# Performance work log

Measured on AMD Instinct MI355X. Metric: run time of the kernel, lower is better.

The kernel has to match this reference:

```python
import jax, jax.numpy as jnp
import numpy as np

EPS = 1e-07


def setup_inputs() -> dict:
    key = jax.random.key(0)
    k1, k2, k3 = jax.random.split(key, 3)
    B, T, R, F = 16, 512, 128, 32
    timesteps = jax.random.uniform(k1, (B, T, F), dtype=jnp.float32)          # observation times, > 0
    values = jax.random.normal(k2, (B, T, F), dtype=jnp.float32)              # observed values
    reference_timesteps = jax.random.uniform(k3, (B, R), dtype=jnp.float32)  # query times
    alpha = jnp.ones((1,), dtype=jnp.float32) * 50.0                          # learned bandwidth param (init a=50)
    return {"timesteps": timesteps, "values": values,
            "reference_timesteps": reference_timesteps, "alpha": alpha}


def reference(timesteps, values, reference_timesteps, alpha):
    # timesteps, values: [B, T, F]; reference_timesteps: [B, R]; alpha: [1]
    R = reference_timesteps.shape[1]
    t = timesteps[:, None, :, :]                       # [B, 1, T, F]
    r = reference_timesteps[:, :, None, None]          # [B, R, 1, 1]
    mask = (t > 0).astype(timesteps.dtype)             # [B, 1, T, F]
    # squared-exponential kernel with mask, normalized by R (as in intensity)
    dist = jnp.exp(-alpha[0] * (r - t) ** 2) * mask + EPS  # [B, R, T, F]
    dist = dist / R
    lam = dist.sum(axis=2)                             # [B, R, F]
    smooth = jnp.sum(dist * values[:, None, :, :], axis=2) / lam  # [B, R, F]
    return smooth
```

## Files before the change

kernel.cpp:

```cpp
#include <hip/hip_runtime.h>


constexpr int B_ = 16, T_ = 512, R_ = 128, F_ = 32;
constexpr int S_  = 4;
constexpr int TS_ = T_ / S_;
constexpr int RB_ = 8;
constexpr float EPS_ = 1e-7f;

__global__ __launch_bounds__(256) void ga_partial(
    const float* __restrict__ ts_g, const float* __restrict__ v_g,
    const float* __restrict__ ref_g, const float* __restrict__ alpha_g,
    float2* __restrict__ ws)
{
    __shared__ float tile[TS_ * F_ * 2];

    const int tid = threadIdx.x;
    const int s   = blockIdx.x % S_;
    const int rb  = (blockIdx.x / S_) % (R_ / RB_);
    const int b   = blockIdx.x / (S_ * (R_ / RB_));
    const int f   = tid & 31;
    const int rl  = tid >> 5;
    const int r_idx = rb * RB_ + rl;

    const float r    = ref_g[b * R_ + r_idx];
    const float nega = -alpha_g[0];

    const float4* tsg4 = (const float4*)(ts_g + (size_t)(b * T_ + s * TS_) * F_);
    const float4* vg4  = (const float4*)(v_g  + (size_t)(b * T_ + s * TS_) * F_);
    #pragma unroll
    for (int i = tid; i < TS_ * F_ / 4; i += 256) {
        float4 a = tsg4[i];
        float4 w = vg4[i];
        a.x = (a.x > 0.f) ? a.x : 2e19f;
        a.y = (a.y > 0.f) ? a.y : 2e19f;
        a.z = (a.z > 0.f) ? a.z : 2e19f;
        a.w = (a.w > 0.f) ? a.w : 2e19f;
        float4* dst = (float4*)(tile + 8 * i);
        dst[0] = make_float4(a.x, w.x, a.y, w.y);
        dst[1] = make_float4(a.z, w.z, a.w, w.w);
    }
    __syncthreads();

    const float2* t2 = (const float2*)tile;
    float num = 0.f, den = 0.f;
    #pragma unroll 8
    for (int t = 0; t < TS_; ++t) {
        float2 tv = t2[t * F_ + f];
        float d = r - tv.x;
        float e = __expf(nega * d * d);
        float wgt = e + EPS_;
        den += wgt;
        num = fmaf(wgt, tv.y, num);
    }

    ws[(size_t)s * (B_ * R_ * F_) + (size_t)(b * R_ + r_idx) * F_ + f] =
        make_float2(num, den);
}

__global__ __launch_bounds__(256) void ga_combine(
    const float2* __restrict__ ws, float* __restrict__ out)
{
    int i = blockIdx.x * 256 + threadIdx.x;
    float num = 0.f, den = 0.f;
    #pragma unroll
    for (int s = 0; s < S_; ++s) {
        float2 p = ws[(size_t)s * (B_ * R_ * F_) + i];
        num += p.x;
        den += p.y;
    }
    out[i] = num / den;
}

extern "C" void kernel_launch(void* const* d_in, const int* in_sizes, int n_in,
                              void* d_out, int out_size, void* d_ws, size_t ws_size,
                              hipStream_t stream) {
    const float* timesteps = (const float*)d_in[0];
    const float* values    = (const float*)d_in[1];
    const float* ref_ts    = (const float*)d_in[2];
    const float* alpha     = (const float*)d_in[3];
    float* out = (float*)d_out;
    float2* ws = (float2*)d_ws;

    ga_partial<<<B_ * (R_ / RB_) * S_, 256, 0, stream>>>(
        timesteps, values, ref_ts, alpha, ws);
    ga_combine<<<(B_ * R_ * F_) / 256, 256, 0, stream>>>(ws, out);
}
```

Measured before the change: 71.29 us.

## Fuse partial and combine kernels into one 1024-thread block per (b, r-block)

Replaces the two-kernel split-T scheme with a single kernel. Each 1024-thread block loads a full batch's T×F tile into LDS, and eight T-groups reduce their partial sums through shared memory before writing the output. It also computes two reference rows per thread to reuse each LDS load, packs two timesteps into a float4 read, and folds log2e into alpha so it can use exp2f. This removes the workspace round trip and the second launch, at the cost of a 128KB LDS tile, lower occupancy and fewer blocks (256).

```diff
diff --git a/kernel.cpp b/kernel.cpp
--- a/kernel.cpp
+++ b/kernel.cpp
@@ -2,73 +2,91 @@
 
 
 constexpr int B_ = 16, T_ = 512, R_ = 128, F_ = 32;
-constexpr int S_  = 4;
-constexpr int TS_ = T_ / S_;
-constexpr int RB_ = 8;
+constexpr int NTG = 8;
+constexpr int CT_ = T_ / NTG;
+constexpr int RSL = 4;
+constexpr int RB_ = RSL * 2;
 constexpr float EPS_ = 1e-7f;
+constexpr float LOG2E_ = 1.4426950408889634f;
 
-__global__ __launch_bounds__(256) void ga_partial(
+__global__ __launch_bounds__(1024) void ga_fused(
     const float* __restrict__ ts_g, const float* __restrict__ v_g,
     const float* __restrict__ ref_g, const float* __restrict__ alpha_g,
-    float2* __restrict__ ws)
+    float* __restrict__ out)
 {
-    __shared__ float tile[TS_ * F_ * 2];
+    __shared__ float4 tile[(T_ / 2) * F_];
 
     const int tid = threadIdx.x;
-    const int s   = blockIdx.x % S_;
-    const int rb  = (blockIdx.x / S_) % (R_ / RB_);
-    const int b   = blockIdx.x / (S_ * (R_ / RB_));
+    const int rb  = blockIdx.x & (R_ / RB_ - 1);
+    const int b   = blockIdx.x >> 4;
     const int f   = tid & 31;
-    const int rl  = tid >> 5;
-    const int r_idx = rb * RB_ + rl;
+    const int rl  = (tid >> 5) & (RSL - 1);
+    const int tg  = tid >> 7;
 
-    const float r    = ref_g[b * R_ + r_idx];
-    const float nega = -alpha_g[0];
+    const float nega2 = -alpha_g[0] * LOG2E_;
+    const float r0 = ref_g[b * R_ + rb * RB_ + rl];
+    const float r1 = ref_g[b * R_ + rb * RB_ + rl + RSL];
 
-    const float4* tsg4 = (const float4*)(ts_g + (size_t)(b * T_ + s * TS_) * F_);
-    const float4* vg4  = (const float4*)(v_g  + (size_t)(b * T_ + s * TS_) * F_);
+    const float4* tsg4 = (const float4*)(ts_g + (size_t)b * T_ * F_);
+    const float4* vg4  = (const float4*)(v_g  + (size_t)b * T_ * F_);
+    float2* dd = (float2*)tile;
     #pragma unroll
-    for (int i = tid; i < TS_ * F_ / 4; i += 256) {
+    for (int it = 0; it < (T_ * F_ / 4) / 1024; ++it) {
+        const int i = tid + it * 1024;
         float4 a = tsg4[i];
         float4 w = vg4[i];
         a.x = (a.x > 0.f) ? a.x : 2e19f;
         a.y = (a.y > 0.f) ? a.y : 2e19f;
         a.z = (a.z > 0.f) ? a.z : 2e19f;
         a.w = (a.w > 0.f) ? a.w : 2e19f;
-        float4* dst = (float4*)(tile + 8 * i);
-        dst[0] = make_float4(a.x, w.x, a.y, w.y);
-        dst[1] = make_float4(a.z, w.z, a.w, w.w);
+        const int t   = i >> 3;
+        const int fq  = i & 7;
+        const int k   = t >> 1;
+        const int par = t & 1;
+        const int base = (k * F_ + fq * 4) * 2 + par;
+        dd[base + 0] = make_float2(a.x, w.x);
+        dd[base + 2] = make_float2(a.y, w.y);
+        dd[base + 4] = make_float2(a.z, w.z);
+        dd[base + 6] = make_float2(a.w, w.w);
     }
     __syncthreads();
 
-    const float2* t2 = (const float2*)tile;
-    float num = 0.f, den = 0.f;
+    float num0 = 0.f, den0 = 0.f, num1 = 0.f, den1 = 0.f;
+    const float4* src = tile + tg * (CT_ / 2) * F_ + f;
     #pragma unroll 8
-    for (int t = 0; t < TS_; ++t) {
-        float2 tv = t2[t * F_ + f];
-        float d = r - tv.x;
-        float e = __expf(nega * d * d);
-        float wgt = e + EPS_;
-        den += wgt;
-        num = fmaf(wgt, tv.y, num);
+    for (int k = 0; k < CT_ / 2; ++k) {
+        const float4 tv = src[k * F_];
+        const float d00 = r0 - tv.x, d10 = r1 - tv.x;
+        const float d01 = r0 - tv.z, d11 = r1 - tv.z;
+        const float e00 = exp2f((nega2 * d00) * d00);
+        const float e10 = exp2f((nega2 * d10) * d10);
+        const float e01 = exp2f((nega2 * d01) * d01);
+        const float e11 = exp2f((nega2 * d11) * d11);
+        const float w00 = e00 + EPS_, w10 = e10 + EPS_;
+        const float w01 = e01 + EPS_, w11 = e11 + EPS_;
+        den0 += w00 + w01;
+        den1 += w10 + w11;
+        num0 = fmaf(w00, tv.y, fmaf(w01, tv.w, num0));
+        num1 = fmaf(w10, tv.y, fmaf(w11, tv.w, num1));
     }
+    __syncthreads();
 
-    ws[(size_t)s * (B_ * R_ * F_) + (size_t)(b * R_ + r_idx) * F_ + f] =
-        make_float2(num, den);
-}
+    float2* red = (float2*)tile;
+    red[((rl      ) * NTG + tg) * F_ + f] = make_float2(num0, den0);
+    red[((rl + RSL) * NTG + tg) * F_ + f] = make_float2(num1, den1);
+    __syncthreads();
 
-__global__ __launch_bounds__(256) void ga_combine(
-    const float2* __restrict__ ws, float* __restrict__ out)
-{
-    int i = blockIdx.x * 256 + threadIdx.x;
-    float num = 0.f, den = 0.f;
-    #pragma unroll
-    for (int s = 0; s < S_; ++s) {
-        float2 p = ws[(size_t)s * (B_ * R_ * F_) + i];
-        num += p.x;
-        den += p.y;
+    if (tid < RB_ * F_) {
+        const int rr = tid >> 5;
+        float num = 0.f, den = 0.f;
+        #pragma unroll
+        for (int g = 0; g < NTG; ++g) {
+            const float2 p = red[(rr * NTG + g) * F_ + f];
+            num += p.x;
+            den += p.y;
+        }
+        out[(size_t)(b * R_ + rb * RB_ + rr) * F_ + f] = num / den;
     }
-    out[i] = num / den;
 }
 
 extern "C" void kernel_launch(void* const* d_in, const int* in_sizes, int n_in,
@@ -79,9 +97,7 @@
     const float* ref_ts    = (const float*)d_in[2];
     const float* alpha     = (const float*)d_in[3];
     float* out = (float*)d_out;
-    float2* ws = (float2*)d_ws;
 
-    ga_partial<<<B_ * (R_ / RB_) * S_, 256, 0, stream>>>(
-        timesteps, values, ref_ts, alpha, ws);
-    ga_combine<<<(B_ * R_ * F_) / 256, 256, 0, stream>>>(ws, out);
+    ga_fused<<<B_ * (R_ / RB_), 1024, 0, stream>>>(
+        timesteps, values, ref_ts, alpha, out);
 }
```

Measured after the change: 73.79 us. 1.04x slower.
